# Optimization experiments

Measured on AMD Instinct MI355X. Metric: run time of the kernel, lower is better.

The kernel has to match this reference:

```python
import jax, jax.numpy as jnp
import numpy as np

N = 8192
E = 262144
D_IN = 768
D_STRUCT = 32
D_HID = 768
D_OUT = 768
MEM_K = 64
MEM_D = 768
NUM_GRAPHS = 64


def setup_inputs() -> dict:
    key = jax.random.key(0)
    ks = jax.random.split(key, 16)
    s = 0.02
    return {
        "feature": jax.random.normal(ks[0], (N, D_IN), jnp.float32),
        "ppr": jax.random.uniform(ks[1], (N,), jnp.float32),
        "edge_attr": jax.random.normal(ks[2], (E, D_IN), jnp.float32),
        "Ws": jax.random.normal(ks[3], (1, D_STRUCT), jnp.float32) * s,
        "bs": jnp.zeros((D_STRUCT,), jnp.float32),
        "W1": jax.random.normal(ks[4], (D_IN + D_STRUCT, D_HID), jnp.float32) * s,
        "b1": jnp.zeros((D_HID,), jnp.float32),
        "prelu_a": jnp.asarray(0.25, jnp.float32),
        "W2": jax.random.normal(ks[5], (D_HID, D_OUT), jnp.float32) * s,
        "b2": jnp.zeros((D_OUT,), jnp.float32),
        "Wp1": jax.random.normal(ks[6], (D_HID, D_HID), jnp.float32) * s,
        "bp1": jnp.zeros((D_HID,), jnp.float32),
        "Wp2": jax.random.normal(ks[7], (D_HID, D_OUT), jnp.float32) * s,
        "bp2": jnp.zeros((D_OUT,), jnp.float32),
        "memory": jax.random.normal(ks[8], (MEM_K, MEM_D), jnp.float32),
        "edge_index": jax.random.randint(ks[9], (2, E), 0, N, jnp.int64),
        "batch_ids": jnp.sort(jax.random.randint(ks[10], (N,), 0, NUM_GRAPHS, jnp.int64)),
        "num_graphs": NUM_GRAPHS,
    }


def reference(feature, ppr, edge_attr, Ws, bs, W1, b1, prelu_a, W2, b2,
              Wp1, bp1, Wp2, bp2, memory, edge_index, batch_ids, num_graphs):
    n = feature.shape[0]
    # aggre_edges: scatter_add edge_attr onto destination nodes (col)
    col = edge_index[1]
    feat = feature + jax.ops.segment_sum(edge_attr, col, num_segments=n)
    # struct encoder: Linear(1, struct_dim) + ReLU on ppr scalar
    struct_feat = jax.nn.relu(ppr[:, None] @ Ws + bs)  # [N, 32]
    # MLP: Linear -> PReLU -> Linear
    h = jnp.concatenate([feat, struct_feat], axis=-1) @ W1 + b1
    h = jnp.where(h > 0, h, prelu_a * h)
    node_feats = h @ W2 + b2  # [N, D_OUT]
    # scatter_mean over graphs
    seg_sum = jax.ops.segment_sum(node_feats, batch_ids, num_segments=num_graphs)
    cnt = jax.ops.segment_sum(jnp.ones((n,), node_feats.dtype), batch_ids, num_segments=num_graphs)
    graph_feats = seg_sum / jnp.maximum(cnt, 1.0)[:, None]
    pooled_feats = jnp.tanh(graph_feats @ Wp1 + bp1) @ Wp2 + bp2
    # memory attention: softmax(M @ nf) over memory slots, then mean(mem_key * M)
    # mean_k(softmax(scores)[n,k] * M[k,d]) == (softmax @ M) / K
    w = jax.nn.softmax(node_feats @ memory.T, axis=1)  # [N, 64]
    re_node_feats = (w @ memory) / memory.shape[0]      # [N, 768]
    loss = jnp.mean((node_feats - re_node_feats) ** 2)
    return pooled_feats, re_node_feats, loss
```

## Files before the change

### kernel.cpp

```cpp
#include <hip/hip_runtime.h>
#include <hip/hip_bf16.h>
#include <math.h>

typedef unsigned short ushort_t;
typedef short bf16x8 __attribute__((ext_vector_type(8)));
typedef float f32x4 __attribute__((ext_vector_type(4)));

#define NNODES   8192
#define DIN      768
#define DSTRUCT  32
#define XDIM     800
#define DHID     768
#define DOUT     768
#define MEMK     64
#define NGRAPH   64
#define BUCKET_CAP 128

#define OFF_XHI     0u
#define OFF_XLO     (OFF_XHI  + 8192u*800u*2u)
#define OFF_HHI     (OFF_XLO  + 8192u*800u*2u)
#define OFF_HLO     (OFF_HHI  + 8192u*768u*2u)
#define OFF_NF      (OFF_HLO  + 8192u*768u*2u)
#define OFF_NFHI    (OFF_NF   + 8192u*768u*4u)
#define OFF_NFLO    (OFF_NFHI + 8192u*768u*2u)
#define OFF_W1THI   (OFF_NFLO + 8192u*768u*2u)
#define OFF_W1TLO   (OFF_W1THI + 768u*800u*2u)
#define OFF_W2THI   (OFF_W1TLO + 768u*800u*2u)
#define OFF_W2TLO   (OFF_W2THI + 768u*768u*2u)
#define OFF_MHI     (OFF_W2TLO + 768u*768u*2u)
#define OFF_MLO     (OFF_MHI  + 64u*768u*2u)
#define OFF_MTHI    (OFF_MLO  + 64u*768u*2u)
#define OFF_MTLO    (OFF_MTHI + 768u*64u*2u)
#define OFF_BUCKET  (OFF_MTLO + 768u*64u*2u)
#define OFF_COUNTS  (OFF_BUCKET + 8192u*BUCKET_CAP*4u)
#define OFF_GSTART  (OFF_COUNTS + 8192u*4u)
#define OFF_GEND    (OFF_GSTART + 256u)
#define OFF_LOSS    (OFF_GEND + 256u)
#define OFF_GFEAT   (OFF_LOSS + 256u)
#define OFF_T1      (OFF_GFEAT + 768u*64u*4u)
#define ZERO_OFF    OFF_COUNTS
#define ZERO_BYTES  (8192u*4u + 256u + 256u + 256u)

__device__ __forceinline__ ushort_t bf_rne(float f) {
    unsigned u = __float_as_uint(f);
    return (ushort_t)((u + 0x7FFFu + ((u >> 16) & 1u)) >> 16);
}
__device__ __forceinline__ void split_bf16(float f, ushort_t& hi, ushort_t& lo) {
    ushort_t h = bf_rne(f);
    float fh = __uint_as_float(((unsigned)h) << 16);
    hi = h;
    lo = bf_rne(f - fh);
}
__device__ __forceinline__ void gld16(const void* g, void* l) {
    __builtin_amdgcn_global_load_lds(
        (const __attribute__((address_space(1))) unsigned int*)g,
        (__attribute__((address_space(3))) unsigned int*)l, 16, 0, 0);
}

__global__ void k_fill_bucket(const int* __restrict__ col, int* __restrict__ counts,
                              int* __restrict__ bucket, int E) {
    for (int e = blockIdx.x * blockDim.x + threadIdx.x; e < E; e += gridDim.x * blockDim.x) {
        int c = col[e];
        if ((unsigned)c < (unsigned)NNODES) {
            int p = atomicAdd(&counts[c], 1);
            if (p < BUCKET_CAP) bucket[c * BUCKET_CAP + p] = e;
        }
    }
}

__global__ __launch_bounds__(192) void k_aggregate(
    const float* __restrict__ feature, const float* __restrict__ edge_attr,
    const float* __restrict__ ppr, const float* __restrict__ Ws, const float* __restrict__ bs,
    const int* __restrict__ bucket, const int* __restrict__ counts,
    ushort_t* __restrict__ Xhi, ushort_t* __restrict__ Xlo) {
    int n = blockIdx.x;
    int t = threadIdx.x;
    const float4* frow = (const float4*)(feature + (size_t)n * DIN);
    float4 acc = frow[t];
    int deg = min(counts[n], BUCKET_CAP);
    const int* bk = bucket + n * BUCKET_CAP;
    for (int j = 0; j < deg; ++j) {
        int e = bk[j];
        float4 v = ((const float4*)(edge_attr + (size_t)e * DIN))[t];
        acc.x += v.x; acc.y += v.y; acc.z += v.z; acc.w += v.w;
    }
    ushort4 h4, l4;
    split_bf16(acc.x, h4.x, l4.x); split_bf16(acc.y, h4.y, l4.y);
    split_bf16(acc.z, h4.z, l4.z); split_bf16(acc.w, h4.w, l4.w);
    *(ushort4*)(Xhi + (size_t)n * XDIM + t * 4) = h4;
    *(ushort4*)(Xlo + (size_t)n * XDIM + t * 4) = l4;
    if (t < DSTRUCT / 4) {
        float p = ppr[n];
        int k = t * 4;
        float4 s;
        s.x = fmaxf(p * Ws[k+0] + bs[k+0], 0.f);
        s.y = fmaxf(p * Ws[k+1] + bs[k+1], 0.f);
        s.z = fmaxf(p * Ws[k+2] + bs[k+2], 0.f);
        s.w = fmaxf(p * Ws[k+3] + bs[k+3], 0.f);
        ushort4 sh, sl;
        split_bf16(s.x, sh.x, sl.x); split_bf16(s.y, sh.y, sl.y);
        split_bf16(s.z, sh.z, sl.z); split_bf16(s.w, sh.w, sl.w);
        *(ushort4*)(Xhi + (size_t)n * XDIM + DIN + k) = sh;
        *(ushort4*)(Xlo + (size_t)n * XDIM + DIN + k) = sl;
    }
}

__global__ __launch_bounds__(256) void k_wsplit(const float* __restrict__ W,
                                                ushort_t* __restrict__ Thi, ushort_t* __restrict__ Tlo,
                                                int K, int N) {
    __shared__ float tile[32][33];
    int n0 = blockIdx.x * 32, k0 = blockIdx.y * 32;
    int tx = threadIdx.x & 31, ty = threadIdx.x >> 5;
#pragma unroll
    for (int i = 0; i < 4; ++i) {
        int k = ty + i * 8;
        tile[k][tx] = W[(size_t)(k0 + k) * N + n0 + tx];
    }
    __syncthreads();
#pragma unroll
    for (int i = 0; i < 4; ++i) {
        int nn = ty + i * 8;
        float v = tile[tx][nn];
        ushort_t hi, lo; split_bf16(v, hi, lo);
        Thi[(size_t)(n0 + nn) * K + k0 + tx] = hi;
        Tlo[(size_t)(n0 + nn) * K + k0 + tx] = lo;
    }
}

__global__ void k_msplit(const float* __restrict__ m, ushort_t* __restrict__ hi,
                         ushort_t* __restrict__ lo, int n) {
    int i = blockIdx.x * 256 + threadIdx.x;
    if (i >= n) return;
    ushort_t h, l; split_bf16(m[i], h, l);
    hi[i] = h; lo[i] = l;
}

#define L_ALO 2048
#define L_BHI 4096
#define L_BLO 8192
#define L_BUF 12288

template<int ACT, int OUTMODE>
__global__ __launch_bounds__(256) void k_gemm_mfma(
    const ushort_t* __restrict__ Ahi, const ushort_t* __restrict__ Alo,
    const ushort_t* __restrict__ Bhi, const ushort_t* __restrict__ Blo,
    const float* __restrict__ bias, const float* __restrict__ act_p,
    float* __restrict__ Cf, ushort_t* __restrict__ Chi, ushort_t* __restrict__ Clo,
    int M, int N, int K) {
    __shared__ ushort_t lds[2 * L_BUF];
    int tid = threadIdx.x;
    int l = tid & 63, w = tid >> 6;

    int nbx = N / 128;
    int nwg = nbx * (M / 64);
    int bid = blockIdx.y * nbx + blockIdx.x;
    int q = nwg >> 3;
    int nb = (bid & 7) * q + (bid >> 3);
    int bx = nb % nbx, by = nb / nbx;
    int m0 = by * 64, n0 = bx * 128;

    int wm = w >> 1, wn = w & 1;

    f32x4 acc[2][4];
#pragma unroll
    for (int m = 0; m < 2; ++m)
#pragma unroll
        for (int n = 0; n < 4; ++n) acc[m][n] = (f32x4){0.f, 0.f, 0.f, 0.f};

    int srow = w * 16 + (l >> 2);
    int sc   = (l & 3) * 8;
    const ushort_t* agh  = Ahi + (size_t)(m0 + srow) * K + sc;
    const ushort_t* agl  = Alo + (size_t)(m0 + srow) * K + sc;
    const ushort_t* bgh0 = Bhi + (size_t)(n0 + srow) * K + sc;
    const ushort_t* bgh1 = Bhi + (size_t)(n0 + 64 + srow) * K + sc;
    const ushort_t* bgl0 = Blo + (size_t)(n0 + srow) * K + sc;
    const ushort_t* bgl1 = Blo + (size_t)(n0 + 64 + srow) * K + sc;

    int NT = K / 32;

    {
        ushort_t* b = lds;
        gld16(agh,  b + w * 512);
        gld16(agl,  b + L_ALO + w * 512);
        gld16(bgh0, b + L_BHI + w * 512);
        gld16(bgh1, b + L_BHI + 2048 + w * 512);
        gld16(bgl0, b + L_BLO + w * 512);
        gld16(bgl1, b + L_BLO + 2048 + w * 512);
    }

    int c0 = l >> 4;
    int arow = wm * 32 + (l & 15);
    int bcol = wn * 64 + (l & 15);

    for (int kt = 0; kt < NT; ++kt) {
        int cur = kt & 1;
        __syncthreads();
        if (kt + 1 < NT) {
            int ko = (kt + 1) * 32;
            ushort_t* b = lds + (cur ^ 1) * L_BUF;
            gld16(agh + ko,  b + w * 512);
            gld16(agl + ko,  b + L_ALO + w * 512);
            gld16(bgh0 + ko, b + L_BHI + w * 512);
            gld16(bgh1 + ko, b + L_BHI + 2048 + w * 512);
            gld16(bgl0 + ko, b + L_BLO + w * 512);
            gld16(bgl1 + ko, b + L_BLO + 2048 + w * 512);
        }
        const ushort_t* cb = lds + cur * L_BUF;
        bf16x8 ah[2], al[2], bh[4], bl[4];
#pragma unroll
        for (int m = 0; m < 2; ++m) {
            ah[m] = *(const bf16x8*)(cb + (arow + m * 16) * 32 + c0 * 8);
            al[m] = *(const bf16x8*)(cb + L_ALO + (arow + m * 16) * 32 + c0 * 8);
        }
#pragma unroll
        for (int n = 0; n < 4; ++n) {
            bh[n] = *(const bf16x8*)(cb + L_BHI + (bcol + n * 16) * 32 + c0 * 8);
            bl[n] = *(const bf16x8*)(cb + L_BLO + (bcol + n * 16) * 32 + c0 * 8);
        }
#pragma unroll
        for (int m = 0; m < 2; ++m)
#pragma unroll
            for (int n = 0; n < 4; ++n) {
                acc[m][n] = __builtin_amdgcn_mfma_f32_16x16x32_bf16(ah[m], bh[n], acc[m][n], 0, 0, 0);
                acc[m][n] = __builtin_amdgcn_mfma_f32_16x16x32_bf16(ah[m], bl[n], acc[m][n], 0, 0, 0);
                acc[m][n] = __builtin_amdgcn_mfma_f32_16x16x32_bf16(al[m], bh[n], acc[m][n], 0, 0, 0);
            }
    }

    float ap = (ACT == 1) ? *act_p : 0.f;
#pragma unroll
    for (int m = 0; m < 2; ++m)
#pragma unroll
        for (int n = 0; n < 4; ++n) {
            int col = n0 + wn * 64 + n * 16 + (l & 15);
            float bv = bias[col];
#pragma unroll
            for (int r = 0; r < 4; ++r) {
                int row = m0 + wm * 32 + m * 16 + (l >> 4) * 4 + r;
                float x = acc[m][n][r] + bv;
                if (ACT == 1) x = x > 0.f ? x : ap * x;
                ushort_t hi, lo; split_bf16(x, hi, lo);
                Chi[(size_t)row * N + col] = hi;
                Clo[(size_t)row * N + col] = lo;
                if (OUTMODE == 2) Cf[(size_t)row * N + col] = x;
            }
        }
}

__global__ void k_boundaries(const int* __restrict__ batch, int* __restrict__ gstart,
                             int* __restrict__ gend, int n) {
    int i = blockIdx.x * blockDim.x + threadIdx.x;
    if (i >= n) return;
    int b = batch[i];
    if ((unsigned)b >= (unsigned)NGRAPH) return;
    if (i == 0 || batch[i - 1] != b) gstart[b] = i;
    if (i == n - 1 || batch[i + 1] != b) gend[b] = i + 1;
}

__global__ __launch_bounds__(128) void k_pool(const float* __restrict__ nf,
                                              const int* __restrict__ gstart, const int* __restrict__ gend,
                                              float* __restrict__ gfeatT) {
    int g = blockIdx.x, d = blockIdx.y * 128 + threadIdx.x;
    int s = gstart[g], e = gend[g];
    float a = 0.f;
    for (int n = s; n < e; ++n) a += nf[(size_t)n * DOUT + d];
    gfeatT[(size_t)d * 64 + g] = a / fmaxf((float)(e - s), 1.f);
}

template<int ACT>
__global__ __launch_bounds__(256) void k_mlp_t(const float* __restrict__ AT, const float* __restrict__ B,
                                               const float* __restrict__ bias,
                                               float* __restrict__ OutT, float* __restrict__ OutR) {
    __shared__ float red[4][64];
    int n = blockIdx.x;
    int l = threadIdx.x & 63, qw = threadIdx.x >> 6;
    float s = 0.f;
    const float* a = AT + l;
    const float* b = B + n;
#pragma unroll 8
    for (int k = qw * 192; k < qw * 192 + 192; ++k)
        s = fmaf(a[k * 64], b[k * 768], s);
    red[qw][l] = s;
    __syncthreads();
    if (threadIdx.x < 64) {
        float v = red[0][l] + red[1][l] + red[2][l] + red[3][l] + bias[n];
        if (ACT == 2) { v = tanhf(v); OutT[n * 64 + l] = v; }
        else OutR[(size_t)l * 768 + n] = v;
    }
}

__global__ __launch_bounds__(256) void k_attn(
    const ushort_t* __restrict__ NFhi, const ushort_t* __restrict__ NFlo,
    const ushort_t* __restrict__ Mhi,  const ushort_t* __restrict__ Mlo,
    const ushort_t* __restrict__ MThi, const ushort_t* __restrict__ MTlo,
    const float* __restrict__ nf, float* __restrict__ re, float* __restrict__ lossac) {
    __shared__ ushort_t Ah[96 * 32 * 8];
    __shared__ ushort_t Al[96 * 32 * 8];
    __shared__ ushort_t Wp[2][32 * 64];
    __shared__ float xch[4][32];
    __shared__ float lred[4];
    int tid = threadIdx.x, l = tid & 63, w = tid >> 6;
    int g = l >> 4, li = l & 15;
    int base = blockIdx.x * 32;

    for (int i = w * 12; i < w * 12 + 12; ++i) {
        int kc = i * 2 + (l >> 5), row = l & 31;
        gld16(NFhi + (size_t)(base + row) * 768 + kc * 8, Ah + i * 512);
        gld16(NFlo + (size_t)(base + row) * 768 + kc * 8, Al + i * 512);
    }
    __syncthreads();

    f32x4 sacc[2];
    sacc[0] = (f32x4){0.f,0.f,0.f,0.f}; sacc[1] = (f32x4){0.f,0.f,0.f,0.f};
    int slot = w * 16 + li;
#pragma unroll 4
    for (int kt = 0; kt < 24; ++kt) {
        bf16x8 ah0 = *(const bf16x8*)(Ah + (kt * 4 + g) * 256 + li * 8);
        bf16x8 ah1 = *(const bf16x8*)(Ah + (kt * 4 + g) * 256 + (li + 16) * 8);
        bf16x8 al0 = *(const bf16x8*)(Al + (kt * 4 + g) * 256 + li * 8);
        bf16x8 al1 = *(const bf16x8*)(Al + (kt * 4 + g) * 256 + (li + 16) * 8);
        bf16x8 bh  = *(const bf16x8*)(Mhi + (size_t)slot * 768 + kt * 32 + g * 8);
        bf16x8 bl  = *(const bf16x8*)(Mlo + (size_t)slot * 768 + kt * 32 + g * 8);
        sacc[0] = __builtin_amdgcn_mfma_f32_16x16x32_bf16(ah0, bh, sacc[0], 0, 0, 0);
        sacc[0] = __builtin_amdgcn_mfma_f32_16x16x32_bf16(ah0, bl, sacc[0], 0, 0, 0);
        sacc[0] = __builtin_amdgcn_mfma_f32_16x16x32_bf16(al0, bh, sacc[0], 0, 0, 0);
        sacc[1] = __builtin_amdgcn_mfma_f32_16x16x32_bf16(ah1, bh, sacc[1], 0, 0, 0);
        sacc[1] = __builtin_amdgcn_mfma_f32_16x16x32_bf16(ah1, bl, sacc[1], 0, 0, 0);
        sacc[1] = __builtin_amdgcn_mfma_f32_16x16x32_bf16(al1, bh, sacc[1], 0, 0, 0);
    }

    float mxv[8];
#pragma unroll
    for (int m = 0; m < 2; ++m)
#pragma unroll
        for (int r = 0; r < 4; ++r) {
            float v = sacc[m][r];
            v = fmaxf(v, __shfl_xor(v, 1)); v = fmaxf(v, __shfl_xor(v, 2));
            v = fmaxf(v, __shfl_xor(v, 4)); v = fmaxf(v, __shfl_xor(v, 8));
            mxv[m * 4 + r] = v;
        }
    if (li == 0) {
#pragma unroll
        for (int m = 0; m < 2; ++m)
#pragma unroll
            for (int r = 0; r < 4; ++r) xch[w][m * 16 + g * 4 + r] = mxv[m * 4 + r];
    }
    __syncthreads();
    float ev[8], sv[8];
#pragma unroll
    for (int m = 0; m < 2; ++m)
#pragma unroll
        for (int r = 0; r < 4; ++r) {
            int row = m * 16 + g * 4 + r;
            float mx = fmaxf(fmaxf(xch[0][row], xch[1][row]), fmaxf(xch[2][row], xch[3][row]));
            float e = __expf(sacc[m][r] - mx);
            ev[m * 4 + r] = e;
            float s = e;
            s += __shfl_xor(s, 1); s += __shfl_xor(s, 2);
            s += __shfl_xor(s, 4); s += __shfl_xor(s, 8);
            sv[m * 4 + r] = s;
        }
    __syncthreads();
    if (li == 0) {
#pragma unroll
        for (int m = 0; m < 2; ++m)
#pragma unroll
            for (int r = 0; r < 4; ++r) xch[w][m * 16 + g * 4 + r] = sv[m * 4 + r];
    }
    __syncthreads();
#pragma unroll
    for (int m = 0; m < 2; ++m)
#pragma unroll
        for (int r = 0; r < 4; ++r) {
            int row = m * 16 + g * 4 + r;
            float tot = xch[0][row] + xch[1][row] + xch[2][row] + xch[3][row];
            float wv = ev[m * 4 + r] / tot;
            ushort_t hi, lo; split_bf16(wv, hi, lo);
            int idx = row * 64 + (slot ^ ((row & 7) << 3));
            Wp[0][idx] = hi; Wp[1][idx] = lo;
        }
    __syncthreads();

    bf16x8 wah[2][2], wal[2][2];
#pragma unroll
    for (int m = 0; m < 2; ++m)
#pragma unroll
        for (int kt2 = 0; kt2 < 2; ++kt2) {
            int row = m * 16 + li;
            int k8 = kt2 * 4 + g;
            int idx = row * 64 + ((k8 * 8) ^ ((row & 7) << 3));
            wah[m][kt2] = *(const bf16x8*)&Wp[0][idx];
            wal[m][kt2] = *(const bf16x8*)&Wp[1][idx];
        }
    float lp = 0.f;
#pragma unroll 2
    for (int nfi = 0; nfi < 12; ++nfi) {
        int col = w * 192 + nfi * 16 + li;
        f32x4 pacc[2];
        pacc[0] = (f32x4){0.f,0.f,0.f,0.f}; pacc[1] = (f32x4){0.f,0.f,0.f,0.f};
#pragma unroll
        for (int kt2 = 0; kt2 < 2; ++kt2) {
            bf16x8 bh = *(const bf16x8*)(MThi + (size_t)col * 64 + kt2 * 32 + g * 8);
            bf16x8 bl = *(const bf16x8*)(MTlo + (size_t)col * 64 + kt2 * 32 + g * 8);
#pragma unroll
            for (int m = 0; m < 2; ++m) {
                pacc[m] = __builtin_amdgcn_mfma_f32_16x16x32_bf16(wah[m][kt2], bh, pacc[m], 0, 0, 0);
                pacc[m] = __builtin_amdgcn_mfma_f32_16x16x32_bf16(wah[m][kt2], bl, pacc[m], 0, 0, 0);
                pacc[m] = __builtin_amdgcn_mfma_f32_16x16x32_bf16(wal[m][kt2], bh, pacc[m], 0, 0, 0);
            }
        }
#pragma unroll
        for (int m = 0; m < 2; ++m)
#pragma unroll
            for (int r = 0; r < 4; ++r) {
                int row = base + m * 16 + g * 4 + r;
                float v = pacc[m][r] * (1.f / 64.f);
                float x = nf[(size_t)row * 768 + col];
                re[(size_t)row * 768 + col] = v;
                float d = x - v;
                lp = fmaf(d, d, lp);
            }
    }
    for (int o = 32; o; o >>= 1) lp += __shfl_xor(lp, o);
    if (l == 0) lred[w] = lp;
    __syncthreads();
    if (tid == 0) atomicAdd(lossac, lred[0] + lred[1] + lred[2] + lred[3]);
}

__global__ void k_loss_final(const float* __restrict__ acc, float* __restrict__ out, float invn) {
    if (threadIdx.x == 0 && blockIdx.x == 0) out[0] = acc[0] * invn;
}

extern "C" void kernel_launch(void* const* d_in, const int* in_sizes, int n_in,
                              void* d_out, int out_size, void* d_ws, size_t ws_size,
                              hipStream_t stream) {
    const float* feature  = (const float*)d_in[0];
    const float* ppr      = (const float*)d_in[1];
    const float* edge_attr= (const float*)d_in[2];
    const float* Ws       = (const float*)d_in[3];
    const float* bs       = (const float*)d_in[4];
    const float* W1       = (const float*)d_in[5];
    const float* b1       = (const float*)d_in[6];
    const float* prelu_a  = (const float*)d_in[7];
    const float* W2       = (const float*)d_in[8];
    const float* b2       = (const float*)d_in[9];
    const float* Wp1      = (const float*)d_in[10];
    const float* bp1      = (const float*)d_in[11];
    const float* Wp2      = (const float*)d_in[12];
    const float* bp2      = (const float*)d_in[13];
    const float* memory   = (const float*)d_in[14];
    const int*   edge_index = (const int*)d_in[15];
    const int*   batch_ids  = (const int*)d_in[16];

    const int E = in_sizes[15] / 2;
    const int N = in_sizes[0] / DIN;
    const int* col = edge_index + E;

    char* ws = (char*)d_ws;
    ushort_t* Xhi  = (ushort_t*)(ws + OFF_XHI);
    ushort_t* Xlo  = (ushort_t*)(ws + OFF_XLO);
    ushort_t* Hhi  = (ushort_t*)(ws + OFF_HHI);
    ushort_t* Hlo  = (ushort_t*)(ws + OFF_HLO);
    float*    nf   = (float*)   (ws + OFF_NF);
    ushort_t* NFhi = (ushort_t*)(ws + OFF_NFHI);
    ushort_t* NFlo = (ushort_t*)(ws + OFF_NFLO);
    ushort_t* W1Thi= (ushort_t*)(ws + OFF_W1THI);
    ushort_t* W1Tlo= (ushort_t*)(ws + OFF_W1TLO);
    ushort_t* W2Thi= (ushort_t*)(ws + OFF_W2THI);
    ushort_t* W2Tlo= (ushort_t*)(ws + OFF_W2TLO);
    ushort_t* Mhi  = (ushort_t*)(ws + OFF_MHI);
    ushort_t* Mlo  = (ushort_t*)(ws + OFF_MLO);
    ushort_t* MThi = (ushort_t*)(ws + OFF_MTHI);
    ushort_t* MTlo = (ushort_t*)(ws + OFF_MTLO);
    int*   bucket = (int*)(ws + OFF_BUCKET);
    int*   counts = (int*)(ws + OFF_COUNTS);
    int*   gstart = (int*)(ws + OFF_GSTART);
    int*   gend   = (int*)(ws + OFF_GEND);
    float* lossac = (float*)(ws + OFF_LOSS);
    float* gfeatT = (float*)(ws + OFF_GFEAT);
    float* t1T    = (float*)(ws + OFF_T1);

    float* out_pooled = (float*)d_out;
    float* out_re     = (float*)d_out + NGRAPH * DOUT;
    float* out_loss   = (float*)d_out + NGRAPH * DOUT + (size_t)N * DOUT;

    (void)hipMemsetAsync(ws + ZERO_OFF, 0, ZERO_BYTES, stream);

    k_wsplit<<<dim3(768 / 32, 800 / 32), 256, 0, stream>>>(W1, W1Thi, W1Tlo, XDIM, DHID);
    k_wsplit<<<dim3(768 / 32, 768 / 32), 256, 0, stream>>>(W2, W2Thi, W2Tlo, DHID, DOUT);
    k_wsplit<<<dim3(768 / 32, 64 / 32), 256, 0, stream>>>(memory, MThi, MTlo, MEMK, DOUT);
    k_msplit<<<(MEMK * 768 + 255) / 256, 256, 0, stream>>>(memory, Mhi, Mlo, MEMK * 768);

    k_fill_bucket<<<1024, 256, 0, stream>>>(col, counts, bucket, E);
    k_aggregate<<<N, 192, 0, stream>>>(feature, edge_attr, ppr, Ws, bs, bucket, counts, Xhi, Xlo);

    k_gemm_mfma<1, 1><<<dim3(DHID / 128, N / 64), 256, 0, stream>>>(
        Xhi, Xlo, W1Thi, W1Tlo, b1, prelu_a, nullptr, Hhi, Hlo, N, DHID, XDIM);
    k_gemm_mfma<0, 2><<<dim3(DOUT / 128, N / 64), 256, 0, stream>>>(
        Hhi, Hlo, W2Thi, W2Tlo, b2, nullptr, nf, NFhi, NFlo, N, DOUT, DHID);

    k_boundaries<<<(N + 255) / 256, 256, 0, stream>>>(batch_ids, gstart, gend, N);
    k_pool<<<dim3(NGRAPH, 6), 128, 0, stream>>>(nf, gstart, gend, gfeatT);

    k_mlp_t<2><<<768, 256, 0, stream>>>(gfeatT, Wp1, bp1, t1T, nullptr);
    k_mlp_t<0><<<768, 256, 0, stream>>>(t1T, Wp2, bp2, nullptr, out_pooled);

    k_attn<<<N / 32, 256, 0, stream>>>(NFhi, NFlo, Mhi, Mlo, MThi, MTlo, nf, out_re, lossac);
    k_loss_final<<<1, 64, 0, stream>>>(lossac, out_loss, 1.f / (float)((size_t)N * DOUT));
}
```

Measured before the change: 414.4 us.

## Merge prep kernels and load GEMM B operand directly from global

The four weight/memory split kernels become one k_prep launch, and the graph-boundary computation is folded into the bucket-fill kernel, cutting the launch count. The MFMA GEMM no longer stages the B (weight) tiles in LDS. Each wave reads its B fragments straight from global/L2, which shrinks LDS per block and adds a launch-bounds occupancy hint. The risk is that the uncoalesced, unprefetched global B loads sit in the inner loop and may stall the MFMAs.

```diff
diff --git a/kernel.cpp b/kernel.cpp
--- a/kernel.cpp
+++ b/kernel.cpp
@@ -57,14 +57,66 @@
         (__attribute__((address_space(3))) unsigned int*)l, 16, 0, 0);
 }
 
+__device__ __forceinline__ void dsplit(const float* __restrict__ W,
+                                       ushort_t* __restrict__ Thi, ushort_t* __restrict__ Tlo,
+                                       int K, int N, int bx, int by) {
+    __shared__ float tile[32][33];
+    int n0 = bx * 32, k0 = by * 32;
+    int tx = threadIdx.x & 31, ty = threadIdx.x >> 5;
+#pragma unroll
+    for (int i = 0; i < 4; ++i) {
+        int k = ty + i * 8;
+        tile[k][tx] = W[(size_t)(k0 + k) * N + n0 + tx];
+    }
+    __syncthreads();
+#pragma unroll
+    for (int i = 0; i < 4; ++i) {
+        int nn = ty + i * 8;
+        float v = tile[tx][nn];
+        ushort_t hi, lo; split_bf16(v, hi, lo);
+        Thi[(size_t)(n0 + nn) * K + k0 + tx] = hi;
+        Tlo[(size_t)(n0 + nn) * K + k0 + tx] = lo;
+    }
+}
+
+__global__ __launch_bounds__(256) void k_prep(
+    const float* __restrict__ W1, const float* __restrict__ W2, const float* __restrict__ mem,
+    ushort_t* __restrict__ W1Thi, ushort_t* __restrict__ W1Tlo,
+    ushort_t* __restrict__ W2Thi, ushort_t* __restrict__ W2Tlo,
+    ushort_t* __restrict__ MThi, ushort_t* __restrict__ MTlo,
+    ushort_t* __restrict__ Mhi, ushort_t* __restrict__ Mlo) {
+    int b = blockIdx.x;
+    if (b < 600)       dsplit(W1, W1Thi, W1Tlo, XDIM, DHID, b % 24, b / 24);
+    else if (b < 1176) dsplit(W2, W2Thi, W2Tlo, DHID, DOUT, (b - 600) % 24, (b - 600) / 24);
+    else if (b < 1224) dsplit(mem, MThi, MTlo, MEMK, DOUT, (b - 1176) % 24, (b - 1176) / 24);
+    else {
+        int i = (b - 1224) * 256 + threadIdx.x;
+        if (i < MEMK * 768) {
+            ushort_t h, l; split_bf16(mem[i], h, l);
+            Mhi[i] = h; Mlo[i] = l;
+        }
+    }
+}
+
 __global__ void k_fill_bucket(const int* __restrict__ col, int* __restrict__ counts,
-                              int* __restrict__ bucket, int E) {
-    for (int e = blockIdx.x * blockDim.x + threadIdx.x; e < E; e += gridDim.x * blockDim.x) {
-        int c = col[e];
-        if ((unsigned)c < (unsigned)NNODES) {
-            int p = atomicAdd(&counts[c], 1);
-            if (p < BUCKET_CAP) bucket[c * BUCKET_CAP + p] = e;
-        }
+                              int* __restrict__ bucket, int E,
+                              const int* __restrict__ batch, int* __restrict__ gstart,
+                              int* __restrict__ gend, int n) {
+    if (blockIdx.x < 1024) {
+        for (int e = blockIdx.x * blockDim.x + threadIdx.x; e < E; e += 1024 * blockDim.x) {
+            int c = col[e];
+            if ((unsigned)c < (unsigned)NNODES) {
+                int p = atomicAdd(&counts[c], 1);
+                if (p < BUCKET_CAP) bucket[c * BUCKET_CAP + p] = e;
+            }
+        }
+    } else {
+        int i = (blockIdx.x - 1024) * 256 + threadIdx.x;
+        if (i >= n) return;
+        int b = batch[i];
+        if ((unsigned)b >= (unsigned)NGRAPH) return;
+        if (i == 0 || batch[i - 1] != b) gstart[b] = i;
+        if (i == n - 1 || batch[i + 1] != b) gend[b] = i + 1;
     }
 }
 
@@ -105,49 +157,17 @@
     }
 }
 
-__global__ __launch_bounds__(256) void k_wsplit(const float* __restrict__ W,
-                                                ushort_t* __restrict__ Thi, ushort_t* __restrict__ Tlo,
-                                                int K, int N) {
-    __shared__ float tile[32][33];
-    int n0 = blockIdx.x * 32, k0 = blockIdx.y * 32;
-    int tx = threadIdx.x & 31, ty = threadIdx.x >> 5;
-#pragma unroll
-    for (int i = 0; i < 4; ++i) {
-        int k = ty + i * 8;
-        tile[k][tx] = W[(size_t)(k0 + k) * N + n0 + tx];
-    }
-    __syncthreads();
-#pragma unroll
-    for (int i = 0; i < 4; ++i) {
-        int nn = ty + i * 8;
-        float v = tile[tx][nn];
-        ushort_t hi, lo; split_bf16(v, hi, lo);
-        Thi[(size_t)(n0 + nn) * K + k0 + tx] = hi;
-        Tlo[(size_t)(n0 + nn) * K + k0 + tx] = lo;
-    }
-}
-
-__global__ void k_msplit(const float* __restrict__ m, ushort_t* __restrict__ hi,
-                         ushort_t* __restrict__ lo, int n) {
-    int i = blockIdx.x * 256 + threadIdx.x;
-    if (i >= n) return;
-    ushort_t h, l; split_bf16(m[i], h, l);
-    hi[i] = h; lo[i] = l;
-}
-
-#define L_ALO 2048
-#define L_BHI 4096
-#define L_BLO 8192
-#define L_BUF 12288
+#define LA_LO  2048
+#define LA_BUF 4096
 
 template<int ACT, int OUTMODE>
-__global__ __launch_bounds__(256) void k_gemm_mfma(
+__global__ __launch_bounds__(256, 4) void k_gemm_mfma(
     const ushort_t* __restrict__ Ahi, const ushort_t* __restrict__ Alo,
     const ushort_t* __restrict__ Bhi, const ushort_t* __restrict__ Blo,
     const float* __restrict__ bias, const float* __restrict__ act_p,
     float* __restrict__ Cf, ushort_t* __restrict__ Chi, ushort_t* __restrict__ Clo,
     int M, int N, int K) {
-    __shared__ ushort_t lds[2 * L_BUF];
+    __shared__ ushort_t lds[2 * LA_BUF];
     int tid = threadIdx.x;
     int l = tid & 63, w = tid >> 6;
 
@@ -169,53 +189,38 @@
 
     int srow = w * 16 + (l >> 2);
     int sc   = (l & 3) * 8;
-    const ushort_t* agh  = Ahi + (size_t)(m0 + srow) * K + sc;
-    const ushort_t* agl  = Alo + (size_t)(m0 + srow) * K + sc;
-    const ushort_t* bgh0 = Bhi + (size_t)(n0 + srow) * K + sc;
-    const ushort_t* bgh1 = Bhi + (size_t)(n0 + 64 + srow) * K + sc;
-    const ushort_t* bgl0 = Blo + (size_t)(n0 + srow) * K + sc;
-    const ushort_t* bgl1 = Blo + (size_t)(n0 + 64 + srow) * K + sc;
+    const ushort_t* agh = Ahi + (size_t)(m0 + srow) * K + sc;
+    const ushort_t* agl = Alo + (size_t)(m0 + srow) * K + sc;
+
+    int c0 = l >> 4, li = l & 15;
+    const ushort_t* bgh = Bhi + (size_t)(n0 + wn * 64 + li) * K + c0 * 8;
+    const ushort_t* bgl = Blo + (size_t)(n0 + wn * 64 + li) * K + c0 * 8;
+
+    gld16(agh, lds + w * 512);
+    gld16(agl, lds + LA_LO + w * 512);
 
     int NT = K / 32;
-
-    {
-        ushort_t* b = lds;
-        gld16(agh,  b + w * 512);
-        gld16(agl,  b + L_ALO + w * 512);
-        gld16(bgh0, b + L_BHI + w * 512);
-        gld16(bgh1, b + L_BHI + 2048 + w * 512);
-        gld16(bgl0, b + L_BLO + w * 512);
-        gld16(bgl1, b + L_BLO + 2048 + w * 512);
-    }
-
-    int c0 = l >> 4;
-    int arow = wm * 32 + (l & 15);
-    int bcol = wn * 64 + (l & 15);
-
     for (int kt = 0; kt < NT; ++kt) {
         int cur = kt & 1;
         __syncthreads();
         if (kt + 1 < NT) {
             int ko = (kt + 1) * 32;
-            ushort_t* b = lds + (cur ^ 1) * L_BUF;
-            gld16(agh + ko,  b + w * 512);
-            gld16(agl + ko,  b + L_ALO + w * 512);
-            gld16(bgh0 + ko, b + L_BHI + w * 512);
-            gld16(bgh1 + ko, b + L_BHI + 2048 + w * 512);
-            gld16(bgl0 + ko, b + L_BLO + w * 512);
-            gld16(bgl1 + ko, b + L_BLO + 2048 + w * 512);
-        }
-        const ushort_t* cb = lds + cur * L_BUF;
+            ushort_t* b = lds + (cur ^ 1) * LA_BUF;
+            gld16(agh + ko, b + w * 512);
+            gld16(agl + ko, b + LA_LO + w * 512);
+        }
+        const ushort_t* cb = lds + cur * LA_BUF;
+        int kb = kt * 32;
         bf16x8 ah[2], al[2], bh[4], bl[4];
 #pragma unroll
+        for (int n = 0; n < 4; ++n) {
+            bh[n] = *(const bf16x8*)(bgh + (size_t)(n * 16) * K + kb);
+            bl[n] = *(const bf16x8*)(bgl + (size_t)(n * 16) * K + kb);
+        }
+#pragma unroll
         for (int m = 0; m < 2; ++m) {
-            ah[m] = *(const bf16x8*)(cb + (arow + m * 16) * 32 + c0 * 8);
-            al[m] = *(const bf16x8*)(cb + L_ALO + (arow + m * 16) * 32 + c0 * 8);
-        }
-#pragma unroll
-        for (int n = 0; n < 4; ++n) {
-            bh[n] = *(const bf16x8*)(cb + L_BHI + (bcol + n * 16) * 32 + c0 * 8);
-            bl[n] = *(const bf16x8*)(cb + L_BLO + (bcol + n * 16) * 32 + c0 * 8);
+            ah[m] = *(const bf16x8*)(cb + (wm * 32 + m * 16 + li) * 32 + c0 * 8);
+            al[m] = *(const bf16x8*)(cb + LA_LO + (wm * 32 + m * 16 + li) * 32 + c0 * 8);
         }
 #pragma unroll
         for (int m = 0; m < 2; ++m)
@@ -245,16 +250,6 @@
                 if (OUTMODE == 2) Cf[(size_t)row * N + col] = x;
             }
         }
-}
-
-__global__ void k_boundaries(const int* __restrict__ batch, int* __restrict__ gstart,
-                             int* __restrict__ gend, int n) {
-    int i = blockIdx.x * blockDim.x + threadIdx.x;
-    if (i >= n) return;
-    int b = batch[i];
-    if ((unsigned)b >= (unsigned)NGRAPH) return;
-    if (i == 0 || batch[i - 1] != b) gstart[b] = i;
-    if (i == n - 1 || batch[i + 1] != b) gend[b] = i + 1;
 }
 
 __global__ __launch_bounds__(128) void k_pool(const float* __restrict__ nf,
@@ -486,12 +481,11 @@
 
     (void)hipMemsetAsync(ws + ZERO_OFF, 0, ZERO_BYTES, stream);
 
-    k_wsplit<<<dim3(768 / 32, 800 / 32), 256, 0, stream>>>(W1, W1Thi, W1Tlo, XDIM, DHID);
-    k_wsplit<<<dim3(768 / 32, 768 / 32), 256, 0, stream>>>(W2, W2Thi, W2Tlo, DHID, DOUT);
-    k_wsplit<<<dim3(768 / 32, 64 / 32), 256, 0, stream>>>(memory, MThi, MTlo, MEMK, DOUT);
-    k_msplit<<<(MEMK * 768 + 255) / 256, 256, 0, stream>>>(memory, Mhi, Mlo, MEMK * 768);
-
-    k_fill_bucket<<<1024, 256, 0, stream>>>(col, counts, bucket, E);
+    k_prep<<<1416, 256, 0, stream>>>(W1, W2, memory, W1Thi, W1Tlo, W2Thi, W2Tlo,
+                                     MThi, MTlo, Mhi, Mlo);
+
+    k_fill_bucket<<<1024 + (NNODES + 255) / 256, 256, 0, stream>>>(
+        col, counts, bucket, E, batch_ids, gstart, gend, N);
     k_aggregate<<<N, 192, 0, stream>>>(feature, edge_attr, ppr, Ws, bs, bucket, counts, Xhi, Xlo);
 
     k_gemm_mfma<1, 1><<<dim3(DHID / 128, N / 64), 256, 0, stream>>>(
@@ -499,7 +493,6 @@
     k_gemm_mfma<0, 2><<<dim3(DOUT / 128, N / 64), 256, 0, stream>>>(
         Hhi, Hlo, W2Thi, W2Tlo, b2, nullptr, nf, NFhi, NFlo, N, DOUT, DHID);
 
-    k_boundaries<<<(N + 255) / 256, 256, 0, stream>>>(batch_ids, gstart, gend, N);
     k_pool<<<dim3(NGRAPH, 6), 128, 0, stream>>>(nf, gstart, gend, gfeatT);
 
     k_mlp_t<2><<<768, 256, 0, stream>>>(gfeatT, Wp1, bp1, t1T, nullptr);
```

Result: slower. 467.8 us (+12.9%).
